# Kernel tuning notes

Measured on AMD Instinct MI355X. Metric: run time of the kernel, lower is better.

## Reference

```python
import jax, jax.numpy as jnp
import numpy as np

OMEGA = 30.0
N = 131072
F = 128   # nodes_per_layer
NB = 3    # n_layers // 2 residual blocks


def setup_inputs() -> dict:
    key = jax.random.key(0)
    ks = jax.random.split(key, 9)
    u = lambda k, shape, lo, hi: jax.random.uniform(k, shape, jnp.float32, lo, hi)
    wb = float(np.sqrt(6.0 / F) / OMEGA)   # SIREN hidden weight bound
    bb = float(1.0 / np.sqrt(F))           # torch default bias bound
    return {
        "coords": jax.random.normal(ks[0], (N, 3), jnp.float32),
        "first_w": u(ks[1], (F, 3), -1.0 / 3.0, 1.0 / 3.0),  # is_first: +-1/in_features
        "first_b": u(ks[2], (F,), -1.0 / float(np.sqrt(3.0)), 1.0 / float(np.sqrt(3.0))),
        "res_w1": u(ks[3], (NB, F, F), -wb, wb),
        "res_b1": u(ks[4], (NB, F), -bb, bb),
        "res_w2": u(ks[5], (NB, F, F), -wb, wb),
        "res_b2": u(ks[6], (NB, F), -bb, bb),
        "final_w": u(ks[7], (4, F), -wb, wb),
        "final_b": u(ks[8], (4,), -bb, bb),
    }


def _net(coords, first_w, first_b, res_w1, res_b1, res_w2, res_b2, final_w, final_b):
    nb = res_w1.shape[0]
    # weight_1 = 0.5 for blocks with i > 0; weight_2 == 1 always for this config
    w1s = jnp.where(jnp.arange(nb) > 0, 0.5, 1.0).astype(coords.dtype)
    h = jnp.sin(OMEGA * (coords @ first_w.T + first_b))  # [N, F]

    def block(h, p):
        w1, b1, w2, b2, s = p
        s1 = jnp.sin(OMEGA * ((s * h) @ w1.T + b1))
        s2 = jnp.sin(OMEGA * (s1 @ w2.T + b2))
        return h + s2, None

    h, _ = jax.lax.scan(block, h, (res_w1, res_b1, res_w2, res_b2, w1s))
    return h @ final_w.T + final_b  # [N, 4]


def reference(coords, first_w, first_b, res_w1, res_b1, res_w2, res_b2, final_w, final_b):
    f = lambda c: _net(c, first_w, first_b, res_w1, res_b1, res_w2, res_b2, final_w, final_b)
    # Per-sample Jacobian d out[:, j] / d coords[:, k] via 3 batched JVPs
    cols = []
    for k in range(3):
        tan = jnp.broadcast_to(jnp.eye(3, dtype=coords.dtype)[k], coords.shape)
        _, jk = jax.jvp(f, (coords,), (tan,))
        cols.append(jk)  # [N, 4]
    J = jnp.stack(cols, axis=-1)  # [N, 4, 3]
    rotation_free = J[:, 0, :]  # grad of scalar potential
    # curl of vector potential (output columns 1:4)
    divergence_free = jnp.stack(
        [
            J[:, 3, 1] - J[:, 2, 2],
            J[:, 1, 2] - J[:, 3, 0],
            J[:, 2, 0] - J[:, 1, 1],
        ],
        axis=1,
    )
    return rotation_free + divergence_free  # [N, 3]
```

## Files before the change

kernel.cpp:

```cpp
#include <hip/hip_runtime.h>
#include <hip/hip_bf16.h>
#include <stdint.h>


#define OMEGA_C 30.0f

constexpr int NPTS = 131072;
constexpr int FDIM = 128;
constexpr int NBLK = 3;
constexpr int P_WG = 16;
constexpr int NTHR = 512;

typedef short bf16x8 __attribute__((ext_vector_type(8)));
typedef float f32x4  __attribute__((ext_vector_type(4)));

__device__ __forceinline__ uint16_t f2bf(float f) {
    __hip_bfloat16 h = __float2bfloat16(f);
    return __builtin_bit_cast(uint16_t, h);
}
__device__ __forceinline__ float bf2f(uint16_t u) {
    return __bfloat162float(__builtin_bit_cast(__hip_bfloat16, u));
}

__device__ __forceinline__ int swz(int row, int col) {
    const int b = col << 1;
    return (row << 8) + ((((b >> 4) ^ (row & 15)) << 4) | (b & 15));
}

__global__ void prep_w_kernel(const float* __restrict__ res_w1,
                              const float* __restrict__ res_w2,
                              uint16_t* __restrict__ ws) {
    const int t = blockIdx.x;
    const int b = t >> 1, l = t & 1;
    const float scale = (l == 0 && b > 0) ? 0.5f : 1.0f;
    const float* src = (l == 0 ? res_w1 : res_w2) + b * FDIM * FDIM;
    uint8_t* dst = reinterpret_cast<uint8_t*>(ws + t * 16384);
    #pragma unroll
    for (int i = 0; i < 8; ++i) {
        const int g   = (int)threadIdx.x + (i << 8);
        const int row = g >> 4, c = g & 15;
        const float4 v0 = *reinterpret_cast<const float4*>(src + (g << 3));
        const float4 v1 = *reinterpret_cast<const float4*>(src + (g << 3) + 4);
        uint4 w;
        w.x = (uint32_t)f2bf(scale * v0.x) | ((uint32_t)f2bf(scale * v0.y) << 16);
        w.y = (uint32_t)f2bf(scale * v0.z) | ((uint32_t)f2bf(scale * v0.w) << 16);
        w.z = (uint32_t)f2bf(scale * v1.x) | ((uint32_t)f2bf(scale * v1.y) << 16);
        w.w = (uint32_t)f2bf(scale * v1.z) | ((uint32_t)f2bf(scale * v1.w) << 16);
        *reinterpret_cast<uint4*>(dst + (row << 8) + ((c ^ (row & 15)) << 4)) = w;
    }
}

__global__ __launch_bounds__(NTHR, 4) void fsrn_kernel(
    const float* __restrict__ coords,
    const float* __restrict__ first_w,
    const float* __restrict__ first_b,
    const float* __restrict__ res_b1,
    const float* __restrict__ res_b2,
    const float* __restrict__ final_w,
    const uint16_t* __restrict__ ws,
    float* __restrict__ out)
{
    __shared__ __align__(16) uint8_t A8[64 * 256];
    __shared__ __align__(16) uint8_t W8[128 * 256];
    __shared__ __align__(16) uint8_t C8[16 * 256];
    __shared__ float xyz[P_WG * 3];
    __shared__ float outp[3][4][P_WG][3];

    const int tid  = threadIdx.x;
    const int wave = tid >> 6;
    const int lane = tid & 63;
    const int l15  = lane & 15;
    const int lq   = lane >> 4;
    const int wm   = wave >> 2;
    const int wn   = wave & 3;
    const int rowbase = wm * 32;
    const int colbase = wn * 32;
    const int pt0  = blockIdx.x * P_WG;

    float mst[2][2][4];
    f32x4 acc[2][2];

    if (tid < P_WG * 3) xyz[tid] = coords[pt0 * 3 + tid];

    auto stageW = [&](int t) {
        const uint4* src = reinterpret_cast<const uint4*>(ws + t * 16384) + tid;
        #pragma unroll
        for (int i = 0; i < 4; ++i)
            *reinterpret_cast<uint4*>(W8 + ((tid + (i << 9)) << 4)) = src[i << 9];
    };

    stageW(0);
    __syncthreads();

    #pragma unroll
    for (int mt = 0; mt < 2; ++mt) {
        const int s_mt = 2*wm + mt;
        #pragma unroll
        for (int nt = 0; nt < 2; ++nt) {
            const int f = colbase + nt*16 + l15;
            const float w0 = first_w[f*3+0], w1 = first_w[f*3+1], w2 = first_w[f*3+2];
            const float fb = first_b[f];
            const float wk = (s_mt == 1) ? w0 : (s_mt == 2) ? w1 : w2;
            #pragma unroll
            for (int j = 0; j < 4; ++j) {
                const int p = lq*4 + j;
                const float pre = OMEGA_C * (xyz[p*3]*w0 + xyz[p*3+1]*w1 + xyz[p*3+2]*w2 + fb);
                const float v = (s_mt == 0) ? __sinf(pre) : OMEGA_C * __cosf(pre) * wk;
                mst[mt][nt][j] = v;
                *reinterpret_cast<uint16_t*>(A8 + swz(rowbase + mt*16 + p, f)) = f2bf(v);
            }
        }
    }
    __syncthreads();

    auto gemm = [&]() {
        #pragma unroll
        for (int mt = 0; mt < 2; ++mt)
            #pragma unroll
            for (int nt = 0; nt < 2; ++nt) acc[mt][nt] = f32x4{0.f,0.f,0.f,0.f};
        #pragma unroll
        for (int kk = 0; kk < 4; ++kk) {
            bf16x8 af0 = *reinterpret_cast<const bf16x8*>(
                A8 + swz(rowbase + l15, kk*32 + lq*8));
            bf16x8 af1 = *reinterpret_cast<const bf16x8*>(
                A8 + swz(rowbase + 16 + l15, kk*32 + lq*8));
            #pragma unroll
            for (int nt = 0; nt < 2; ++nt) {
                const bf16x8 wf = *reinterpret_cast<const bf16x8*>(
                    W8 + swz(colbase + nt*16 + l15, kk*32 + lq*8));
                acc[0][nt] = __builtin_amdgcn_mfma_f32_16x16x32_bf16(af0, wf, acc[0][nt], 0, 0, 0);
                acc[1][nt] = __builtin_amdgcn_mfma_f32_16x16x32_bf16(af1, wf, acc[1][nt], 0, 0, 0);
            }
        }
    };

    #pragma unroll 1
    for (int b = 0; b < NBLK; ++b) {
        gemm();
        if (wm == 0) {
            #pragma unroll
            for (int nt = 0; nt < 2; ++nt) {
                const int f = colbase + nt*16 + l15;
                const float ob = OMEGA_C * res_b1[b*FDIM + f];
                #pragma unroll
                for (int j = 0; j < 4; ++j) {
                    const int p = lq*4 + j;
                    const float pre = OMEGA_C * acc[0][nt][j] + ob;
                    float sv, cv;
                    __sincosf(pre, &sv, &cv);
                    *reinterpret_cast<uint16_t*>(C8 + swz(p, f)) = f2bf(OMEGA_C * cv);
                    acc[0][nt][j] = sv;
                }
            }
        }
        __syncthreads();
        if (wm == 0) {
            #pragma unroll
            for (int nt = 0; nt < 2; ++nt) {
                const int f = colbase + nt*16 + l15;
                #pragma unroll
                for (int j = 0; j < 4; ++j) {
                    const int p = lq*4 + j;
                    *reinterpret_cast<uint16_t*>(A8 + swz(p, f)) = f2bf(acc[0][nt][j]);
                    const float cv = bf2f(*reinterpret_cast<const uint16_t*>(C8 + swz(p, f)));
                    *reinterpret_cast<uint16_t*>(A8 + swz(16 + p, f)) = f2bf(cv * acc[1][nt][j]);
                }
            }
        } else {
            #pragma unroll
            for (int mt = 0; mt < 2; ++mt)
                #pragma unroll
                for (int nt = 0; nt < 2; ++nt) {
                    const int f = colbase + nt*16 + l15;
                    #pragma unroll
                    for (int j = 0; j < 4; ++j) {
                        const int p = lq*4 + j;
                        const float cv = bf2f(*reinterpret_cast<const uint16_t*>(C8 + swz(p, f)));
                        *reinterpret_cast<uint16_t*>(A8 + swz(rowbase + mt*16 + p, f))
                            = f2bf(cv * acc[mt][nt][j]);
                    }
                }
        }
        stageW(2*b + 1);
        __syncthreads();

        gemm();
        if (wm == 0) {
            #pragma unroll
            for (int nt = 0; nt < 2; ++nt) {
                const int f = colbase + nt*16 + l15;
                const float ob = OMEGA_C * res_b2[b*FDIM + f];
                #pragma unroll
                for (int j = 0; j < 4; ++j) {
                    const int p = lq*4 + j;
                    const float pre = OMEGA_C * acc[0][nt][j] + ob;
                    float sv, cv;
                    __sincosf(pre, &sv, &cv);
                    *reinterpret_cast<uint16_t*>(C8 + swz(p, f)) = f2bf(OMEGA_C * cv);
                    mst[0][nt][j] += sv;
                    acc[0][nt][j] = mst[0][nt][j];
                }
            }
        }
        __syncthreads();
        if (wm == 0) {
            #pragma unroll
            for (int nt = 0; nt < 2; ++nt) {
                const int f = colbase + nt*16 + l15;
                #pragma unroll
                for (int j = 0; j < 4; ++j) {
                    const int p = lq*4 + j;
                    *reinterpret_cast<uint16_t*>(A8 + swz(p, f)) = f2bf(acc[0][nt][j]);
                    const float cv = bf2f(*reinterpret_cast<const uint16_t*>(C8 + swz(p, f)));
                    mst[1][nt][j] += cv * acc[1][nt][j];
                    *reinterpret_cast<uint16_t*>(A8 + swz(16 + p, f)) = f2bf(mst[1][nt][j]);
                }
            }
        } else {
            #pragma unroll
            for (int mt = 0; mt < 2; ++mt)
                #pragma unroll
                for (int nt = 0; nt < 2; ++nt) {
                    const int f = colbase + nt*16 + l15;
                    #pragma unroll
                    for (int j = 0; j < 4; ++j) {
                        const int p = lq*4 + j;
                        const float cv = bf2f(*reinterpret_cast<const uint16_t*>(C8 + swz(p, f)));
                        mst[mt][nt][j] += cv * acc[mt][nt][j];
                        *reinterpret_cast<uint16_t*>(A8 + swz(rowbase + mt*16 + p, f))
                            = f2bf(mst[mt][nt][j]);
                    }
                }
        }
        if (b < NBLK-1) stageW(2*b + 2);
        __syncthreads();
    }

    #pragma unroll
    for (int mt = 0; mt < 2; ++mt) {
        if (wm == 1 || mt == 1) {
            const int k = 2*wm + mt - 1;
            #pragma unroll
            for (int c = 0; c < 3; ++c) {
                int wr; float sg;
                if (c == 0)      { wr = (k==0)?0:(k==1)?3:2; sg = (k==2)?-1.f:1.f; }
                else if (c == 1) { wr = (k==0)?3:(k==1)?0:1; sg = (k==0)?-1.f:1.f; }
                else             { wr = (k==0)?2:(k==1)?1:0; sg = (k==1)?-1.f:1.f; }
                const float fw0 = final_w[wr*FDIM + colbase + l15];
                const float fw1 = final_w[wr*FDIM + colbase + 16 + l15];
                #pragma unroll
                for (int j = 0; j < 4; ++j) {
                    float part = mst[mt][0][j] * fw0 + mst[mt][1][j] * fw1;
                    part += __shfl_xor(part, 1);
                    part += __shfl_xor(part, 2);
                    part += __shfl_xor(part, 4);
                    part += __shfl_xor(part, 8);
                    if (l15 == 0) outp[k][wn][lq*4 + j][c] = sg * part;
                }
            }
        }
    }
    __syncthreads();

    if (tid < P_WG * 3) {
        const int p = tid / 3, c = tid % 3;
        float s = 0.f;
        #pragma unroll
        for (int k = 0; k < 3; ++k)
            #pragma unroll
            for (int q = 0; q < 4; ++q) s += outp[k][q][p][c];
        out[(pt0 + p)*3 + c] = s;
    }
}

extern "C" void kernel_launch(void* const* d_in, const int* in_sizes, int n_in,
                              void* d_out, int out_size, void* d_ws, size_t ws_size,
                              hipStream_t stream) {
    const float* coords  = (const float*)d_in[0];
    const float* first_w = (const float*)d_in[1];
    const float* first_b = (const float*)d_in[2];
    const float* res_w1  = (const float*)d_in[3];
    const float* res_b1  = (const float*)d_in[4];
    const float* res_w2  = (const float*)d_in[5];
    const float* res_b2  = (const float*)d_in[6];
    const float* final_w = (const float*)d_in[7];
    uint16_t* ws = (uint16_t*)d_ws;

    prep_w_kernel<<<dim3(6), dim3(256), 0, stream>>>(res_w1, res_w2, ws);
    fsrn_kernel<<<dim3(NPTS / P_WG), dim3(NTHR), 0, stream>>>(
        coords, first_w, first_b, res_b1, res_b2, final_w, ws, (float*)d_out);
}
```

Before: 353.0 us.

## Load MFMA weight fragments directly from global memory in fragment order

The prep kernel now writes bf16 weights pre-arranged in the exact per-lane MFMA B-fragment order, so each wave reads its fragments with coalesced 16-byte global loads inside the GEMM. This removes the 32KB shared-memory weight buffer, the per-layer staging copies, and the LDS reads of weights, which cuts LDS use and should let more workgroups fit per CU. The cost is that each GEMM now waits on global or L2 loads with little prefetch ahead of the MFMAs. The weights are small and shared by all blocks, so they should stay cache-resident.

```diff
diff --git a/kernel.cpp b/kernel.cpp
--- a/kernel.cpp
+++ b/kernel.cpp
@@ -29,24 +29,28 @@
 
 __global__ void prep_w_kernel(const float* __restrict__ res_w1,
                               const float* __restrict__ res_w2,
-                              uint16_t* __restrict__ ws) {
+                              uint4* __restrict__ ws) {
     const int t = blockIdx.x;
     const int b = t >> 1, l = t & 1;
     const float scale = (l == 0 && b > 0) ? 0.5f : 1.0f;
     const float* src = (l == 0 ? res_w1 : res_w2) + b * FDIM * FDIM;
-    uint8_t* dst = reinterpret_cast<uint8_t*>(ws + t * 16384);
     #pragma unroll
     for (int i = 0; i < 8; ++i) {
-        const int g   = (int)threadIdx.x + (i << 8);
-        const int row = g >> 4, c = g & 15;
-        const float4 v0 = *reinterpret_cast<const float4*>(src + (g << 3));
-        const float4 v1 = *reinterpret_cast<const float4*>(src + (g << 3) + 4);
+        const int g    = (int)threadIdx.x + (i << 8);
+        const int lane = g & 63;
+        const int nt   = (g >> 6) & 1;
+        const int kk   = (g >> 7) & 3;
+        const int wn   = g >> 9;
+        const int col  = wn*32 + nt*16 + (lane & 15);
+        const int k0   = kk*32 + (lane >> 4) * 8;
+        const float4 v0 = *reinterpret_cast<const float4*>(src + col*FDIM + k0);
+        const float4 v1 = *reinterpret_cast<const float4*>(src + col*FDIM + k0 + 4);
         uint4 w;
-        w.x = (uint32_t)f2bf(scale * v0.x) | ((uint32_t)f2bf(scale * v0.y) << 16);
-        w.y = (uint32_t)f2bf(scale * v0.z) | ((uint32_t)f2bf(scale * v0.w) << 16);
-        w.z = (uint32_t)f2bf(scale * v1.x) | ((uint32_t)f2bf(scale * v1.y) << 16);
-        w.w = (uint32_t)f2bf(scale * v1.z) | ((uint32_t)f2bf(scale * v1.w) << 16);
-        *reinterpret_cast<uint4*>(dst + (row << 8) + ((c ^ (row & 15)) << 4)) = w;
+        w.x = (uint32_t)f2bf(scale*v0.x) | ((uint32_t)f2bf(scale*v0.y) << 16);
+        w.y = (uint32_t)f2bf(scale*v0.z) | ((uint32_t)f2bf(scale*v0.w) << 16);
+        w.z = (uint32_t)f2bf(scale*v1.x) | ((uint32_t)f2bf(scale*v1.y) << 16);
+        w.w = (uint32_t)f2bf(scale*v1.z) | ((uint32_t)f2bf(scale*v1.w) << 16);
+        ws[t*2048 + g] = w;
     }
 }
 
@@ -57,11 +61,10 @@
     const float* __restrict__ res_b1,
     const float* __restrict__ res_b2,
     const float* __restrict__ final_w,
-    const uint16_t* __restrict__ ws,
+    const uint4* __restrict__ ws,
     float* __restrict__ out)
 {
     __shared__ __align__(16) uint8_t A8[64 * 256];
-    __shared__ __align__(16) uint8_t W8[128 * 256];
     __shared__ __align__(16) uint8_t C8[16 * 256];
     __shared__ float xyz[P_WG * 3];
     __shared__ float outp[3][4][P_WG][3];
@@ -81,15 +84,6 @@
     f32x4 acc[2][2];
 
     if (tid < P_WG * 3) xyz[tid] = coords[pt0 * 3 + tid];
-
-    auto stageW = [&](int t) {
-        const uint4* src = reinterpret_cast<const uint4*>(ws + t * 16384) + tid;
-        #pragma unroll
-        for (int i = 0; i < 4; ++i)
-            *reinterpret_cast<uint4*>(W8 + ((tid + (i << 9)) << 4)) = src[i << 9];
-    };
-
-    stageW(0);
     __syncthreads();
 
     #pragma unroll
@@ -113,30 +107,32 @@
     }
     __syncthreads();
 
-    auto gemm = [&]() {
+    auto gemm = [&](int t) {
         #pragma unroll
         for (int mt = 0; mt < 2; ++mt)
             #pragma unroll
             for (int nt = 0; nt < 2; ++nt) acc[mt][nt] = f32x4{0.f,0.f,0.f,0.f};
+        const uint4* wbase = ws + (t*4 + wn)*512 + lane;
         #pragma unroll
         for (int kk = 0; kk < 4; ++kk) {
-            bf16x8 af0 = *reinterpret_cast<const bf16x8*>(
+            const uint4 wq0 = wbase[kk*128];
+            const uint4 wq1 = wbase[kk*128 + 64];
+            const bf16x8 wf0 = __builtin_bit_cast(bf16x8, wq0);
+            const bf16x8 wf1 = __builtin_bit_cast(bf16x8, wq1);
+            const bf16x8 af0 = *reinterpret_cast<const bf16x8*>(
                 A8 + swz(rowbase + l15, kk*32 + lq*8));
-            bf16x8 af1 = *reinterpret_cast<const bf16x8*>(
+            const bf16x8 af1 = *reinterpret_cast<const bf16x8*>(
                 A8 + swz(rowbase + 16 + l15, kk*32 + lq*8));
-            #pragma unroll
-            for (int nt = 0; nt < 2; ++nt) {
-                const bf16x8 wf = *reinterpret_cast<const bf16x8*>(
-                    W8 + swz(colbase + nt*16 + l15, kk*32 + lq*8));
-                acc[0][nt] = __builtin_amdgcn_mfma_f32_16x16x32_bf16(af0, wf, acc[0][nt], 0, 0, 0);
-                acc[1][nt] = __builtin_amdgcn_mfma_f32_16x16x32_bf16(af1, wf, acc[1][nt], 0, 0, 0);
-            }
+            acc[0][0] = __builtin_amdgcn_mfma_f32_16x16x32_bf16(af0, wf0, acc[0][0], 0, 0, 0);
+            acc[0][1] = __builtin_amdgcn_mfma_f32_16x16x32_bf16(af0, wf1, acc[0][1], 0, 0, 0);
+            acc[1][0] = __builtin_amdgcn_mfma_f32_16x16x32_bf16(af1, wf0, acc[1][0], 0, 0, 0);
+            acc[1][1] = __builtin_amdgcn_mfma_f32_16x16x32_bf16(af1, wf1, acc[1][1], 0, 0, 0);
         }
     };
 
     #pragma unroll 1
     for (int b = 0; b < NBLK; ++b) {
-        gemm();
+        gemm(2*b);
         if (wm == 0) {
             #pragma unroll
             for (int nt = 0; nt < 2; ++nt) {
@@ -181,10 +177,9 @@
                     }
                 }
         }
-        stageW(2*b + 1);
-        __syncthreads();
-
-        gemm();
+        __syncthreads();
+
+        gemm(2*b + 1);
         if (wm == 0) {
             #pragma unroll
             for (int nt = 0; nt < 2; ++nt) {
@@ -232,7 +227,6 @@
                     }
                 }
         }
-        if (b < NBLK-1) stageW(2*b + 2);
         __syncthreads();
     }
 
@@ -284,7 +278,7 @@
     const float* res_w2  = (const float*)d_in[5];
     const float* res_b2  = (const float*)d_in[6];
     const float* final_w = (const float*)d_in[7];
-    uint16_t* ws = (uint16_t*)d_ws;
+    uint4* ws = (uint4*)d_ws;
 
     prep_w_kernel<<<dim3(6), dim3(256), 0, stream>>>(res_w1, res_w2, ws);
     fsrn_kernel<<<dim3(NPTS / P_WG), dim3(NTHR), 0, stream>>>(
```

New measurement: 327.4 us. -7.3%, faster.
